# Performance work log

Measured on AMD Instinct MI355X. Metric: run time of the kernel, lower is better.

The kernel has to match this reference:

```python
import jax, jax.numpy as jnp
import numpy as np

HEADS = 16
DIM_HEAD = 64
EPS = 1e-5


def _layernorm(x, w, b):
    mu = jnp.mean(x, axis=-1, keepdims=True)
    var = jnp.var(x, axis=-1, keepdims=True)
    return (x - mu) * jax.lax.rsqrt(var + EPS) * w + b


def setup_inputs() -> dict:
    key = jax.random.key(0)
    ks = jax.random.split(key, 6)
    B, F, Q, D = 8, 4096, 64, 1024
    inner = HEADS * DIM_HEAD  # 1024
    s = 0.02
    return {
        "features": jax.random.normal(ks[0], (B, F, D), jnp.float32),
        "latents": jax.random.normal(ks[1], (B, Q, D), jnp.float32),
        "lnm_w": jnp.ones((D,), jnp.float32),
        "lnm_b": jnp.zeros((D,), jnp.float32),
        "lnl_w": jnp.ones((D,), jnp.float32),
        "lnl_b": jnp.zeros((D,), jnp.float32),
        "Wq": jax.random.normal(ks[2], (D, inner), jnp.float32) * s,
        "Wk": jax.random.normal(ks[3], (D, inner), jnp.float32) * s,
        "Wv": jax.random.normal(ks[4], (D, inner), jnp.float32) * s,
        "Wo": jax.random.normal(ks[5], (inner, D), jnp.float32) * s,
    }


def reference(features, latents, lnm_w, lnm_b, lnl_w, lnl_b, Wq, Wk, Wv, Wo):
    B, Q = latents.shape[0], latents.shape[1]
    scale = DIM_HEAD ** (-0.5)

    x = _layernorm(features, lnm_w, lnm_b)           # (B, F, D)
    lat = _layernorm(latents, lnl_w, lnl_b)          # (B, Q, D)

    q = (lat @ Wq).reshape(B, Q, HEADS, DIM_HEAD).transpose(0, 2, 1, 3)  # b h q d
    kv_in = jnp.concatenate([x, lat], axis=1)        # (B, F+Q, D)
    FL = kv_in.shape[1]
    k = (kv_in @ Wk).reshape(B, FL, HEADS, DIM_HEAD).transpose(0, 2, 1, 3)  # b h f d
    v = (kv_in @ Wv).reshape(B, FL, HEADS, DIM_HEAD).transpose(0, 2, 1, 3)  # b h f d

    sim = jnp.einsum('bhqd,bhfd->bhqf', q * scale, k)
    alphas = jax.nn.softmax(sim, axis=-1)            # amax-subtract is folded into stable softmax
    out = jnp.einsum('bhqf,bhfv->bhqv', alphas, v)
    out = out.transpose(0, 2, 1, 3).reshape(B, Q, HEADS * DIM_HEAD)
    return out @ Wo
```

## Files before the change

kernel.cpp:

```cpp
#include <hip/hip_runtime.h>


typedef float   f32x4  __attribute__((ext_vector_type(4)));
typedef short   bf16x8 __attribute__((ext_vector_type(8)));

#define MFMA_BF16 __builtin_amdgcn_mfma_f32_16x16x32_bf16

__device__ __forceinline__ unsigned short f2bf(float f) {
  unsigned u = __float_as_uint(f);
  unsigned r = (u + 0x7fffu + ((u >> 16) & 1u)) >> 16;
  return (unsigned short)r;
}

__device__ __forceinline__ void gload_lds16(const unsigned short* g, unsigned short* l) {
  __builtin_amdgcn_global_load_lds(
      (const __attribute__((address_space(1))) unsigned int*)g,
      (__attribute__((address_space(3))) unsigned int*)l, 16, 0, 0);
}

__global__ __launch_bounds__(256) void ln_kernel(
    const float* __restrict__ features, const float* __restrict__ latents,
    const float* __restrict__ lnm_w, const float* __restrict__ lnm_b,
    const float* __restrict__ lnl_w, const float* __restrict__ lnl_b,
    unsigned short* __restrict__ kv_ln, unsigned short* __restrict__ lat_ln)
{
  const int row = blockIdx.x;
  const int b  = row / 4160;
  const int fi = row - b * 4160;
  const bool is_lat = fi >= 4096;
  const float* x = is_lat ? (latents + (size_t)(b * 64 + fi - 4096) * 1024)
                          : (features + (size_t)(b * 4096 + fi) * 1024);
  const float* wp = is_lat ? lnl_w : lnm_w;
  const float* bp = is_lat ? lnl_b : lnm_b;
  const int tid = threadIdx.x;

  float4 v = *(const float4*)(x + tid * 4);
  float s  = v.x + v.y + v.z + v.w;
  float s2 = v.x * v.x + v.y * v.y + v.z * v.z + v.w * v.w;
#pragma unroll
  for (int sh = 1; sh < 64; sh <<= 1) {
    s  += __shfl_xor(s,  sh, 64);
    s2 += __shfl_xor(s2, sh, 64);
  }
  __shared__ float red[8];
  if ((tid & 63) == 0) { red[tid >> 6] = s; red[4 + (tid >> 6)] = s2; }
  __syncthreads();
  s  = red[0] + red[1] + red[2] + red[3];
  s2 = red[4] + red[5] + red[6] + red[7];
  const float mu   = s * (1.0f / 1024.0f);
  const float var  = s2 * (1.0f / 1024.0f) - mu * mu;
  const float rstd = rsqrtf(var + 1e-5f);

  float4 w4 = *(const float4*)(wp + tid * 4);
  float4 b4 = *(const float4*)(bp + tid * 4);
  ushort4 o;
  o.x = f2bf((v.x - mu) * rstd * w4.x + b4.x);
  o.y = f2bf((v.y - mu) * rstd * w4.y + b4.y);
  o.z = f2bf((v.z - mu) * rstd * w4.z + b4.z);
  o.w = f2bf((v.w - mu) * rstd * w4.w + b4.w);
  *(ushort4*)(kv_ln + (size_t)row * 1024 + tid * 4) = o;
  if (is_lat)
    *(ushort4*)(lat_ln + (size_t)(b * 64 + fi - 4096) * 1024 + tid * 4) = o;
}

__global__ __launch_bounds__(256) void wcast_kernel(
    const float* __restrict__ Wq, const float* __restrict__ Wk,
    const float* __restrict__ Wv, const float* __restrict__ Wo,
    unsigned short* __restrict__ Wkv_t, unsigned short* __restrict__ Wq_t,
    unsigned short* __restrict__ Wo_t)
{
  __shared__ float tile[32][33];
  const int kt = blockIdx.x * 32, nt = blockIdx.y * 32;
  const int tx = threadIdx.x & 31, ty = threadIdx.x >> 5;

  const float* src; int nc; float scale = 1.0f;
  if (nt < 1024)      { src = Wk; nc = nt; }
  else if (nt < 2048) { src = Wv; nc = nt - 1024; }
  else if (nt < 3072) { src = Wq; nc = nt - 2048; scale = 0.125f; }
  else                { src = Wo; nc = nt - 3072; }

#pragma unroll
  for (int kk = 0; kk < 4; ++kk)
    tile[ty + kk * 8][tx] = src[(size_t)(kt + ty + kk * 8) * 1024 + nc + tx] * scale;
  __syncthreads();

#pragma unroll
  for (int nn = 0; nn < 4; ++nn) {
    const int ng = nt + ty + nn * 8;
    unsigned short* d;
    if (ng < 2048)      d = Wkv_t + (size_t)ng * 1024;
    else if (ng < 3072) d = Wq_t + (size_t)(ng - 2048) * 1024;
    else                d = Wo_t + (size_t)(ng - 3072) * 1024;
    d[kt + tx] = f2bf(tile[tx][ty + nn * 8]);
  }
}

__global__ __launch_bounds__(512, 2) void gemm256_bf16(
    const unsigned short* __restrict__ A,
    const unsigned short* __restrict__ Bt,
    unsigned short* __restrict__ C, int M, int N, int K)
{
  __shared__ __align__(16) unsigned short lds[65536];
  const int tid  = threadIdx.x;
  const int wave = tid >> 6, lane = tid & 63;
  const int lo = lane & 15, hi = lane >> 4;
  const int wr = wave >> 2, wc = wave & 3;

  const int nbn = gridDim.x;
  int flat = blockIdx.y * nbn + blockIdx.x;
  const int nwg = nbn * gridDim.y;
  flat = (flat & 7) * (nwg >> 3) + (flat >> 3);
  const int bm = flat / nbn, bn = flat - bm * nbn;

  int roff[2], coff[2];
#pragma unroll
  for (int g = 0; g < 2; ++g) {
    int off = g * 8192 + tid * 16;
    int p = off ^ (((off >> 9) & 1) << 5);
    int sub = (p >> 10) & 15;
    int q = p & 1023;
    roff[g] = ((sub >> 1) << 4) + (q >> 6);
    coff[g] = ((sub & 1) << 5) + ((q & 63) >> 1);
  }
  const unsigned short* pA[2];
  const unsigned short* pB[2];
#pragma unroll
  for (int g = 0; g < 2; ++g) {
    pA[g] = A  + (size_t)(bm * 256 + roff[g]) * K + coff[g];
    pB[g] = Bt + (size_t)(bn * 256 + roff[g]) * K + coff[g];
  }
  const int halfStep = 128 * K;

  f32x4 acc[8][4];
#pragma unroll
  for (int i = 0; i < 8; ++i)
#pragma unroll
    for (int j = 0; j < 4; ++j) acc[i][j] = (f32x4){0.f, 0.f, 0.f, 0.f};

  const int NT = K >> 6;

#pragma unroll
  for (int ty = 0; ty < 4; ++ty) {
#pragma unroll
    for (int g = 0; g < 2; ++g) {
      const unsigned short* src = (ty == 0) ? pA[g]
                                : (ty == 1) ? pB[g]
                                : (ty == 2) ? pA[g] + halfStep
                                            : pB[g] + halfStep;
      gload_lds16(src, lds + ty * 8192 + g * 4096 + wave * 512);
    }
  }
  asm volatile("s_waitcnt vmcnt(6)" ::: "memory");
  asm volatile("s_barrier" ::: "memory");

  bf16x8 aLo[4][2], aHi[4][2], bLo[2][2], bHi[2][2];
  const int swz = (lo * 32 + hi * 8) ^ ((lo & 8) << 1);

#pragma unroll 2
  for (int t = 0; t < NT; ++t) {
    const unsigned short* sb = lds + (t & 1) * 32768;
    unsigned short*       db = lds + ((t + 1) & 1) * 32768;
    const int k0n = (t + 1) << 6;
    const bool st = (t + 1 < NT);

#pragma unroll
    for (int m = 0; m < 4; ++m)
#pragma unroll
      for (int ks = 0; ks < 2; ++ks)
        aLo[m][ks] = *(const bf16x8*)(sb + ((wr * 4 + m) * 2 + ks) * 512 + swz);
    if (st) {
#pragma unroll
      for (int g = 0; g < 2; ++g)
        gload_lds16(pA[g] + k0n, db + g * 4096 + wave * 512);
    }
    asm volatile("s_barrier" ::: "memory");
    asm volatile("s_waitcnt lgkmcnt(0)" ::: "memory");
    __builtin_amdgcn_sched_barrier(0);
    __builtin_amdgcn_s_setprio(1);
    if (t > 0) {
#pragma unroll
      for (int m = 0; m < 4; ++m)
#pragma unroll
        for (int n = 0; n < 2; ++n)
#pragma unroll
          for (int ks = 0; ks < 2; ++ks)
            acc[4 + m][2 + n] = MFMA_BF16(aHi[m][ks], bHi[n][ks], acc[4 + m][2 + n], 0, 0, 0);
    }
    __builtin_amdgcn_s_setprio(0);
    if (st) { asm volatile("s_waitcnt vmcnt(6)" ::: "memory"); }
    else    { asm volatile("s_waitcnt vmcnt(4)" ::: "memory"); }
    asm volatile("s_barrier" ::: "memory");

#pragma unroll
    for (int n = 0; n < 2; ++n)
#pragma unroll
      for (int ks = 0; ks < 2; ++ks)
        bLo[n][ks] = *(const bf16x8*)(sb + 8192 + ((wc * 2 + n) * 2 + ks) * 512 + swz);
    if (st) {
#pragma unroll
      for (int g = 0; g < 2; ++g)
        gload_lds16(pB[g] + k0n, db + 8192 + g * 4096 + wave * 512);
    }
    asm volatile("s_barrier" ::: "memory");
    asm volatile("s_waitcnt lgkmcnt(0)" ::: "memory");
    __builtin_amdgcn_sched_barrier(0);
    __builtin_amdgcn_s_setprio(1);
#pragma unroll
    for (int m = 0; m < 4; ++m)
#pragma unroll
      for (int n = 0; n < 2; ++n)
#pragma unroll
        for (int ks = 0; ks < 2; ++ks)
          acc[m][n] = MFMA_BF16(aLo[m][ks], bLo[n][ks], acc[m][n], 0, 0, 0);
    __builtin_amdgcn_s_setprio(0);
    if (st) { asm volatile("s_waitcnt vmcnt(6)" ::: "memory"); }
    else    { asm volatile("s_waitcnt vmcnt(2)" ::: "memory"); }
    asm volatile("s_barrier" ::: "memory");

#pragma unroll
    for (int m = 0; m < 4; ++m)
#pragma unroll
      for (int ks = 0; ks < 2; ++ks)
        aHi[m][ks] = *(const bf16x8*)(sb + 16384 + ((wr * 4 + m) * 2 + ks) * 512 + swz);
    if (st) {
#pragma unroll
      for (int g = 0; g < 2; ++g)
        gload_lds16(pA[g] + halfStep + k0n, db + 16384 + g * 4096 + wave * 512);
    }
    asm volatile("s_barrier" ::: "memory");
    asm volatile("s_waitcnt lgkmcnt(0)" ::: "memory");
    __builtin_amdgcn_sched_barrier(0);
    __builtin_amdgcn_s_setprio(1);
#pragma unroll
    for (int m = 0; m < 4; ++m)
#pragma unroll
      for (int n = 0; n < 2; ++n)
#pragma unroll
        for (int ks = 0; ks < 2; ++ks)
          acc[4 + m][n] = MFMA_BF16(aHi[m][ks], bLo[n][ks], acc[4 + m][n], 0, 0, 0);
    __builtin_amdgcn_s_setprio(0);
    if (st) { asm volatile("s_waitcnt vmcnt(6)" ::: "memory"); }
    else    { asm volatile("s_waitcnt vmcnt(0)" ::: "memory"); }
    asm volatile("s_barrier" ::: "memory");

#pragma unroll
    for (int n = 0; n < 2; ++n)
#pragma unroll
      for (int ks = 0; ks < 2; ++ks)
        bHi[n][ks] = *(const bf16x8*)(sb + 24576 + ((wc * 2 + n) * 2 + ks) * 512 + swz);
    if (st) {
#pragma unroll
      for (int g = 0; g < 2; ++g)
        gload_lds16(pB[g] + halfStep + k0n, db + 24576 + g * 4096 + wave * 512);
    }
    asm volatile("s_barrier" ::: "memory");
    asm volatile("s_waitcnt lgkmcnt(0)" ::: "memory");
    __builtin_amdgcn_sched_barrier(0);
    __builtin_amdgcn_s_setprio(1);
#pragma unroll
    for (int m = 0; m < 4; ++m)
#pragma unroll
      for (int n = 0; n < 2; ++n)
#pragma unroll
        for (int ks = 0; ks < 2; ++ks)
          acc[m][2 + n] = MFMA_BF16(aLo[m][ks], bHi[n][ks], acc[m][2 + n], 0, 0, 0);
    __builtin_amdgcn_s_setprio(0);
    if (st) { asm volatile("s_waitcnt vmcnt(6)" ::: "memory"); }
    asm volatile("s_barrier" ::: "memory");
  }

#pragma unroll
  for (int m = 0; m < 4; ++m)
#pragma unroll
    for (int n = 0; n < 2; ++n)
#pragma unroll
      for (int ks = 0; ks < 2; ++ks)
        acc[4 + m][2 + n] = MFMA_BF16(aHi[m][ks], bHi[n][ks], acc[4 + m][2 + n], 0, 0, 0);

#pragma unroll
  for (int i = 0; i < 8; ++i) {
    const int grow0 = bm * 256 + (i >> 2) * 128 + wr * 64 + (i & 3) * 16 + hi * 4;
#pragma unroll
    for (int j = 0; j < 4; ++j) {
      const int gcol = bn * 256 + (j >> 1) * 128 + wc * 32 + (j & 1) * 16 + lo;
#pragma unroll
      for (int r = 0; r < 4; ++r)
        C[(size_t)(grow0 + r) * N + gcol] = f2bf(acc[i][j][r]);
    }
  }
}

template <typename CT>
__global__ __launch_bounds__(256) void gemm_tn(
    const unsigned short* __restrict__ A,
    const unsigned short* __restrict__ Bt,
    CT* __restrict__ C, int M, int N, int K)
{
  __shared__ __align__(16) unsigned short sA[2][128 * 32];
  __shared__ __align__(16) unsigned short sB[2][128 * 32];
  const int tid  = threadIdx.x;
  const int wave = tid >> 6, lane = tid & 63;
  const int bm = blockIdx.y, bn = blockIdx.x;
  const int wr = wave >> 1, wc = wave & 1;
  const int lo = lane & 15, hi = lane >> 4;
  const int srow = lane >> 2, squad = lane & 3;

  const unsigned short* gA = A  + (size_t)(bm * 128 + srow) * K + squad * 8;
  const unsigned short* gB = Bt + (size_t)(bn * 128 + srow) * K + squad * 8;

  f32x4 acc[4][4];
#pragma unroll
  for (int i = 0; i < 4; ++i)
#pragma unroll
    for (int j = 0; j < 4; ++j) acc[i][j] = (f32x4){0.f, 0.f, 0.f, 0.f};

  const int kt = K >> 5;
#pragma unroll
  for (int c = 0; c < 2; ++c) {
    const int chunk = wave * 2 + c;
    gload_lds16(gA + (size_t)chunk * 16 * K, &sA[0][chunk * 512]);
    gload_lds16(gB + (size_t)chunk * 16 * K, &sB[0][chunk * 512]);
  }
  __syncthreads();

  int buf = 0;
  for (int t = 0; t < kt; ++t) {
    if (t + 1 < kt) {
      const int k0 = (t + 1) << 5;
#pragma unroll
      for (int c = 0; c < 2; ++c) {
        const int chunk = wave * 2 + c;
        gload_lds16(gA + (size_t)chunk * 16 * K + k0, &sA[buf ^ 1][chunk * 512]);
        gload_lds16(gB + (size_t)chunk * 16 * K + k0, &sB[buf ^ 1][chunk * 512]);
      }
    }
    bf16x8 af[4], bfr[4];
#pragma unroll
    for (int i = 0; i < 4; ++i) {
      af[i]  = *(const bf16x8*)&sA[buf][(wr * 64 + i * 16 + lo) * 32 + hi * 8];
      bfr[i] = *(const bf16x8*)&sB[buf][(wc * 64 + i * 16 + lo) * 32 + hi * 8];
    }
#pragma unroll
    for (int i = 0; i < 4; ++i)
#pragma unroll
      for (int j = 0; j < 4; ++j)
        acc[i][j] = MFMA_BF16(af[i], bfr[j], acc[i][j], 0, 0, 0);
    __syncthreads();
    buf ^= 1;
  }

#pragma unroll
  for (int i = 0; i < 4; ++i) {
    const int row0 = bm * 128 + wr * 64 + i * 16 + hi * 4;
#pragma unroll
    for (int j = 0; j < 4; ++j) {
      const int col = bn * 128 + wc * 64 + j * 16 + lo;
#pragma unroll
      for (int r = 0; r < 4; ++r) {
        const size_t idx = (size_t)(row0 + r) * N + col;
        if constexpr (sizeof(CT) == 2) C[idx] = (CT)f2bf(acc[i][j][r]);
        else                            C[idx] = acc[i][j][r];
      }
    }
  }
}

__global__ __launch_bounds__(256) void attn_kernel(
    const unsigned short* __restrict__ qws,
    const unsigned short* __restrict__ KV,
    float* __restrict__ pacc, float* __restrict__ pml)
{
  const int bhs = blockIdx.x;
  const int s = bhs & 3, h = (bhs >> 2) & 15, b = bhs >> 6;
  const int t0 = (s * 65) >> 2;
  const int t1 = ((s + 1) * 65) >> 2;
  const int tid = threadIdx.x;
  const int wave = tid >> 6, lane = tid & 63;
  const int lo = lane & 15, hi = lane >> 4;

  __shared__ __align__(16) unsigned short sK [64][72];
  __shared__ __align__(16) unsigned short sVT[64][72];
  __shared__ __align__(16) unsigned short sP [4][16][72];

  bf16x8 qf[2];
  {
    const unsigned short* p = qws + (size_t)(b * 64 + wave * 16 + lo) * 1024 + h * 64 + hi * 8;
    qf[0] = *(const bf16x8*)p;
    qf[1] = *(const bf16x8*)(p + 32);
  }
  float m[4] = {-1e30f, -1e30f, -1e30f, -1e30f};
  float l[4] = {0.f, 0.f, 0.f, 0.f};
  f32x4 acc[4];
#pragma unroll
  for (int i = 0; i < 4; ++i) acc[i] = (f32x4){0.f, 0.f, 0.f, 0.f};

  const int frow = tid >> 2, c4 = tid & 3;

  bf16x8 kreg[2], vreg[2];
  {
    const size_t rb = (size_t)(b * 4160 + t0 * 64 + frow) * 2048 + h * 64;
#pragma unroll
    for (int rr = 0; rr < 2; ++rr) {
      const int d0 = rr * 32 + c4 * 8;
      kreg[rr] = *(const bf16x8*)(KV + rb + d0);
      vreg[rr] = *(const bf16x8*)(KV + rb + 1024 + d0);
    }
  }

  for (int t = t0; t < t1; ++t) {
    __syncthreads();
#pragma unroll
    for (int rr = 0; rr < 2; ++rr) {
      const int d0 = rr * 32 + c4 * 8;
      *(bf16x8*)&sK[frow][d0] = kreg[rr];
#pragma unroll
      for (int j = 0; j < 8; ++j) sVT[d0 + j][frow] = (unsigned short)vreg[rr][j];
    }
    __syncthreads();
    if (t + 1 < t1) {
      const size_t rb = (size_t)(b * 4160 + (t + 1) * 64 + frow) * 2048 + h * 64;
#pragma unroll
      for (int rr = 0; rr < 2; ++rr) {
        const int d0 = rr * 32 + c4 * 8;
        kreg[rr] = *(const bf16x8*)(KV + rb + d0);
        vreg[rr] = *(const bf16x8*)(KV + rb + 1024 + d0);
      }
    }

    f32x4 sim[4];
#pragma unroll
    for (int nf = 0; nf < 4; ++nf) {
      f32x4 a0 = (f32x4){0.f, 0.f, 0.f, 0.f};
#pragma unroll
      for (int ks = 0; ks < 2; ++ks) {
        bf16x8 kf = *(const bf16x8*)&sK[nf * 16 + lo][ks * 32 + hi * 8];
        a0 = MFMA_BF16(qf[ks], kf, a0, 0, 0, 0);
      }
      sim[nf] = a0;
    }

    float pr[4][4];
    float corr[4];
#pragma unroll
    for (int r = 0; r < 4; ++r) {
      float tm = fmaxf(fmaxf(sim[0][r], sim[1][r]), fmaxf(sim[2][r], sim[3][r]));
#pragma unroll
      for (int sh = 1; sh < 16; sh <<= 1) tm = fmaxf(tm, __shfl_xor(tm, sh, 64));
      const float mn = fmaxf(m[r], tm);
      corr[r] = __expf(m[r] - mn);
      float rs = 0.f;
#pragma unroll
      for (int nf = 0; nf < 4; ++nf) {
        float p = __expf(sim[nf][r] - mn);
        pr[r][nf] = p;
        rs += p;
      }
#pragma unroll
      for (int sh = 1; sh < 16; sh <<= 1) rs += __shfl_xor(rs, sh, 64);
      l[r] = l[r] * corr[r] + rs;
      m[r] = mn;
    }

    {
      const int r2 = lane & 3;
      float csel = r2 == 0 ? corr[0] : r2 == 1 ? corr[1] : r2 == 2 ? corr[2] : corr[3];
      const int src = ((lane & 15) >> 2) * 16 + (lane & 3);
      const float cacc = __shfl(csel, src, 64);
#pragma unroll
      for (int i = 0; i < 4; ++i) acc[i] *= cacc;
    }

#pragma unroll
    for (int r = 0; r < 4; ++r)
#pragma unroll
      for (int nf = 0; nf < 4; ++nf)
        sP[wave][hi * 4 + r][nf * 16 + lo] = f2bf(pr[r][nf]);

#pragma unroll
    for (int ks = 0; ks < 2; ++ks) {
      bf16x8 pf = *(const bf16x8*)&sP[wave][lo][ks * 32 + hi * 8];
#pragma unroll
      for (int i = 0; i < 4; ++i) {
        bf16x8 vf = *(const bf16x8*)&sVT[i * 16 + lo][ks * 32 + hi * 8];
        acc[i] = MFMA_BF16(vf, pf, acc[i], 0, 0, 0);
      }
    }
  }

  if (lo == 0) {
#pragma unroll
    for (int r = 0; r < 4; ++r) {
      pml[bhs * 128 + wave * 16 + hi * 4 + r]      = m[r];
      pml[bhs * 128 + 64 + wave * 16 + hi * 4 + r] = l[r];
    }
  }
#pragma unroll
  for (int i = 0; i < 4; ++i)
#pragma unroll
    for (int r = 0; r < 4; ++r)
      pacc[bhs * 4096 + (i * 16 + hi * 4 + r) * 64 + wave * 16 + lo] = acc[i][r];
}

__global__ __launch_bounds__(256) void attn_combine(
    const float* __restrict__ pacc, const float* __restrict__ pml,
    unsigned short* __restrict__ attn_out)
{
  const int bh = blockIdx.x;
  const int b = bh >> 4, h = bh & 15;
  const int t = threadIdx.x;
  const int q = t & 63, dg = t >> 6;
  const int base = bh << 2;

  float mm[4], ll[4];
#pragma unroll
  for (int s = 0; s < 4; ++s) {
    mm[s] = pml[(base + s) * 128 + q];
    ll[s] = pml[(base + s) * 128 + 64 + q];
  }
  float M = fmaxf(fmaxf(mm[0], mm[1]), fmaxf(mm[2], mm[3]));
  float e[4];
  float L = 0.f;
#pragma unroll
  for (int s = 0; s < 4; ++s) { e[s] = __expf(mm[s] - M); L += e[s] * ll[s]; }
  const float inv = 1.0f / L;

#pragma unroll
  for (int dd = 0; dd < 16; ++dd) {
    const int d = dg * 16 + dd;
    float v = 0.f;
#pragma unroll
    for (int s = 0; s < 4; ++s)
      v += e[s] * pacc[(base + s) * 4096 + d * 64 + q];
    attn_out[(size_t)(b * 64 + q) * 1024 + h * 64 + d] = f2bf(v * inv);
  }
}

extern "C" void kernel_launch(void* const* d_in, const int* in_sizes, int n_in,
                              void* d_out, int out_size, void* d_ws, size_t ws_size,
                              hipStream_t stream) {
  const float* features = (const float*)d_in[0];
  const float* latents  = (const float*)d_in[1];
  const float* lnm_w = (const float*)d_in[2];
  const float* lnm_b = (const float*)d_in[3];
  const float* lnl_w = (const float*)d_in[4];
  const float* lnl_b = (const float*)d_in[5];
  const float* Wq = (const float*)d_in[6];
  const float* Wk = (const float*)d_in[7];
  const float* Wv = (const float*)d_in[8];
  const float* Wo = (const float*)d_in[9];
  float* out = (float*)d_out;

  char* ws = (char*)d_ws;
  unsigned short* kv_ln    = (unsigned short*)(ws);
  unsigned short* Wkv_t    = (unsigned short*)(ws + 68157440);
  unsigned short* Wq_t     = (unsigned short*)(ws + 72351744);
  unsigned short* Wo_t     = (unsigned short*)(ws + 74448896);
  unsigned short* lat_ln   = (unsigned short*)(ws + 76546048);
  unsigned short* q_ws     = (unsigned short*)(ws + 77594624);
  unsigned short* attn_out = (unsigned short*)(ws + 78643200);
  unsigned short* KV       = (unsigned short*)(ws + 79691776);
  float* pacc = (float*)(ws);
  float* pml  = (float*)(ws + 8388608);

  ln_kernel<<<33280, 256, 0, stream>>>(features, latents, lnm_w, lnm_b, lnl_w, lnl_b,
                                       kv_ln, lat_ln);
  wcast_kernel<<<dim3(32, 128), 256, 0, stream>>>(Wq, Wk, Wv, Wo, Wkv_t, Wq_t, Wo_t);
  gemm256_bf16<<<dim3(8, 130), 512, 0, stream>>>(kv_ln, Wkv_t, KV, 33280, 2048, 1024);
  gemm_tn<unsigned short><<<dim3(8, 4), 256, 0, stream>>>(lat_ln, Wq_t, q_ws, 512, 1024, 1024);
  attn_kernel<<<512, 256, 0, stream>>>(q_ws, KV, pacc, pml);
  attn_combine<<<128, 256, 0, stream>>>(pacc, pml, attn_out);
  gemm_tn<float><<<dim3(8, 4), 256, 0, stream>>>(attn_out, Wo_t, out, 512, 1024, 1024);
}
```

Baseline: 292.9 us.

## Make KV projection GEMM persistent with per-XCD tile ownership and continuous pipeline

The big KV projection GEMM now launches a fixed grid of 256 persistent workgroups instead of one per output tile. Each workgroup walks a strided sequence of tiles that belong to its XCD, stepping 4 tile-rows at a time. The double-buffered K loop runs straight across tile boundaries, so prefetch of the next tile overlaps the epilogue of the current one. This targets the 1040-tile tail-wave imbalance and the per-tile pipeline ramp, at the cost of more complex indexing and an epilogue store inside the main loop that can stall the pipeline.

After: 294.0 us. About the same (+0.3%).

```diff
diff --git a/kernel.cpp b/kernel.cpp
--- a/kernel.cpp
+++ b/kernel.cpp
@@ -106,30 +106,35 @@
   const int lo = lane & 15, hi = lane >> 4;
   const int wr = wave >> 2, wc = wave & 3;
 
-  const int nbn = gridDim.x;
-  int flat = blockIdx.y * nbn + blockIdx.x;
-  const int nwg = nbn * gridDim.y;
-  flat = (flat & 7) * (nwg >> 3) + (flat >> 3);
-  const int bm = flat / nbn, bn = flat - bm * nbn;
+  const int tilesN = N >> 8;
+  const int perXcd = ((M >> 8) * tilesN) >> 3;
+  const int xcd = blockIdx.x & 7, slot = blockIdx.x >> 3;
+  const int ntw = (perXcd - slot + 31) >> 5;
+  const int KT  = (K >> 6) * ntw;
+
+  int g = xcd * perXcd + slot;
+  int bm = g / tilesN;
+  const int bn = g - bm * tilesN;
 
   int roff[2], coff[2];
 #pragma unroll
-  for (int g = 0; g < 2; ++g) {
-    int off = g * 8192 + tid * 16;
+  for (int gi = 0; gi < 2; ++gi) {
+    int off = gi * 8192 + tid * 16;
     int p = off ^ (((off >> 9) & 1) << 5);
     int sub = (p >> 10) & 15;
     int q = p & 1023;
-    roff[g] = ((sub >> 1) << 4) + (q >> 6);
-    coff[g] = ((sub & 1) << 5) + ((q & 63) >> 1);
+    roff[gi] = ((sub >> 1) << 4) + (q >> 6);
+    coff[gi] = ((sub & 1) << 5) + ((q & 63) >> 1);
   }
   const unsigned short* pA[2];
   const unsigned short* pB[2];
 #pragma unroll
-  for (int g = 0; g < 2; ++g) {
-    pA[g] = A  + (size_t)(bm * 256 + roff[g]) * K + coff[g];
-    pB[g] = Bt + (size_t)(bn * 256 + roff[g]) * K + coff[g];
-  }
-  const int halfStep = 128 * K;
+  for (int gi = 0; gi < 2; ++gi) {
+    pA[gi] = A  + (size_t)(bm * 256 + roff[gi]) * K + coff[gi];
+    pB[gi] = Bt + (size_t)(bn * 256 + roff[gi]) * K + coff[gi];
+  }
+  const int halfStep  = 128 * K;
+  const int tileStepA = 4 * 256 * K;
 
   f32x4 acc[8][4];
 #pragma unroll
@@ -137,17 +142,15 @@
 #pragma unroll
     for (int j = 0; j < 4; ++j) acc[i][j] = (f32x4){0.f, 0.f, 0.f, 0.f};
 
-  const int NT = K >> 6;
-
 #pragma unroll
   for (int ty = 0; ty < 4; ++ty) {
 #pragma unroll
-    for (int g = 0; g < 2; ++g) {
-      const unsigned short* src = (ty == 0) ? pA[g]
-                                : (ty == 1) ? pB[g]
-                                : (ty == 2) ? pA[g] + halfStep
-                                            : pB[g] + halfStep;
-      gload_lds16(src, lds + ty * 8192 + g * 4096 + wave * 512);
+    for (int gi = 0; gi < 2; ++gi) {
+      const unsigned short* src = (ty == 0) ? pA[gi]
+                                : (ty == 1) ? pB[gi]
+                                : (ty == 2) ? pA[gi] + halfStep
+                                            : pB[gi] + halfStep;
+      gload_lds16(src, lds + ty * 8192 + gi * 4096 + wave * 512);
     }
   }
   asm volatile("s_waitcnt vmcnt(6)" ::: "memory");
@@ -156,12 +159,14 @@
   bf16x8 aLo[4][2], aHi[4][2], bLo[2][2], bHi[2][2];
   const int swz = (lo * 32 + hi * 8) ^ ((lo & 8) << 1);
 
-#pragma unroll 2
-  for (int t = 0; t < NT; ++t) {
-    const unsigned short* sb = lds + (t & 1) * 32768;
-    unsigned short*       db = lds + ((t + 1) & 1) * 32768;
-    const int k0n = (t + 1) << 6;
-    const bool st = (t + 1 < NT);
+  for (int kt = 0; kt < KT; ++kt) {
+    const int t_local = kt & 15;
+    const bool bnd = (t_local == 15);
+    const bool st  = (kt + 1 < KT);
+    const unsigned short* sb = lds + (kt & 1) * 32768;
+    unsigned short*       db = lds + ((kt + 1) & 1) * 32768;
+    const int offA = bnd ? tileStepA : ((t_local + 1) << 6);
+    const int offB = bnd ? 0         : ((t_local + 1) << 6);
 
 #pragma unroll
     for (int m = 0; m < 4; ++m)
@@ -170,14 +175,14 @@
         aLo[m][ks] = *(const bf16x8*)(sb + ((wr * 4 + m) * 2 + ks) * 512 + swz);
     if (st) {
 #pragma unroll
-      for (int g = 0; g < 2; ++g)
-        gload_lds16(pA[g] + k0n, db + g * 4096 + wave * 512);
+      for (int gi = 0; gi < 2; ++gi)
+        gload_lds16(pA[gi] + offA, db + gi * 4096 + wave * 512);
     }
     asm volatile("s_barrier" ::: "memory");
     asm volatile("s_waitcnt lgkmcnt(0)" ::: "memory");
     __builtin_amdgcn_sched_barrier(0);
     __builtin_amdgcn_s_setprio(1);
-    if (t > 0) {
+    if (t_local != 0) {
 #pragma unroll
       for (int m = 0; m < 4; ++m)
 #pragma unroll
@@ -198,8 +203,8 @@
         bLo[n][ks] = *(const bf16x8*)(sb + 8192 + ((wc * 2 + n) * 2 + ks) * 512 + swz);
     if (st) {
 #pragma unroll
-      for (int g = 0; g < 2; ++g)
-        gload_lds16(pB[g] + k0n, db + 8192 + g * 4096 + wave * 512);
+      for (int gi = 0; gi < 2; ++gi)
+        gload_lds16(pB[gi] + offB, db + 8192 + gi * 4096 + wave * 512);
     }
     asm volatile("s_barrier" ::: "memory");
     asm volatile("s_waitcnt lgkmcnt(0)" ::: "memory");
@@ -224,8 +229,8 @@
         aHi[m][ks] = *(const bf16x8*)(sb + 16384 + ((wr * 4 + m) * 2 + ks) * 512 + swz);
     if (st) {
 #pragma unroll
-      for (int g = 0; g < 2; ++g)
-        gload_lds16(pA[g] + halfStep + k0n, db + 16384 + g * 4096 + wave * 512);
+      for (int gi = 0; gi < 2; ++gi)
+        gload_lds16(pA[gi] + offA + halfStep, db + 16384 + gi * 4096 + wave * 512);
     }
     asm volatile("s_barrier" ::: "memory");
     asm volatile("s_waitcnt lgkmcnt(0)" ::: "memory");
@@ -250,8 +255,8 @@
         bHi[n][ks] = *(const bf16x8*)(sb + 24576 + ((wc * 2 + n) * 2 + ks) * 512 + swz);
     if (st) {
 #pragma unroll
-      for (int g = 0; g < 2; ++g)
-        gload_lds16(pB[g] + halfStep + k0n, db + 24576 + g * 4096 + wave * 512);
+      for (int gi = 0; gi < 2; ++gi)
+        gload_lds16(pB[gi] + offB + halfStep, db + 24576 + gi * 4096 + wave * 512);
     }
     asm volatile("s_barrier" ::: "memory");
     asm volatile("s_waitcnt lgkmcnt(0)" ::: "memory");
@@ -267,25 +272,35 @@
     __builtin_amdgcn_s_setprio(0);
     if (st) { asm volatile("s_waitcnt vmcnt(6)" ::: "memory"); }
     asm volatile("s_barrier" ::: "memory");
-  }
-
-#pragma unroll
-  for (int m = 0; m < 4; ++m)
-#pragma unroll
-    for (int n = 0; n < 2; ++n)
-#pragma unroll
-      for (int ks = 0; ks < 2; ++ks)
-        acc[4 + m][2 + n] = MFMA_BF16(aHi[m][ks], bHi[n][ks], acc[4 + m][2 + n], 0, 0, 0);
-
-#pragma unroll
-  for (int i = 0; i < 8; ++i) {
-    const int grow0 = bm * 256 + (i >> 2) * 128 + wr * 64 + (i & 3) * 16 + hi * 4;
-#pragma unroll
-    for (int j = 0; j < 4; ++j) {
-      const int gcol = bn * 256 + (j >> 1) * 128 + wc * 32 + (j & 1) * 16 + lo;
-#pragma unroll
-      for (int r = 0; r < 4; ++r)
-        C[(size_t)(grow0 + r) * N + gcol] = f2bf(acc[i][j][r]);
+
+    if (bnd) {
+#pragma unroll
+      for (int m = 0; m < 4; ++m)
+#pragma unroll
+        for (int n = 0; n < 2; ++n)
+#pragma unroll
+          for (int ks = 0; ks < 2; ++ks)
+            acc[4 + m][2 + n] = MFMA_BF16(aHi[m][ks], bHi[n][ks], acc[4 + m][2 + n], 0, 0, 0);
+
+#pragma unroll
+      for (int i = 0; i < 8; ++i) {
+        const int grow0 = bm * 256 + (i >> 2) * 128 + wr * 64 + (i & 3) * 16 + hi * 4;
+#pragma unroll
+        for (int j = 0; j < 4; ++j) {
+          const int gcol = bn * 256 + (j >> 1) * 128 + wc * 32 + (j & 1) * 16 + lo;
+#pragma unroll
+          for (int r = 0; r < 4; ++r)
+            C[(size_t)(grow0 + r) * N + gcol] = f2bf(acc[i][j][r]);
+        }
+      }
+#pragma unroll
+      for (int i = 0; i < 8; ++i)
+#pragma unroll
+        for (int j = 0; j < 4; ++j) acc[i][j] = (f32x4){0.f, 0.f, 0.f, 0.f};
+      if (st) {
+        pA[0] += tileStepA; pA[1] += tileStepA;
+        bm += 4;
+      }
     }
   }
 }
@@ -565,7 +580,7 @@
   ln_kernel<<<33280, 256, 0, stream>>>(features, latents, lnm_w, lnm_b, lnl_w, lnl_b,
                                        kv_ln, lat_ln);
   wcast_kernel<<<dim3(32, 128), 256, 0, stream>>>(Wq, Wk, Wv, Wo, Wkv_t, Wq_t, Wo_t);
-  gemm256_bf16<<<dim3(8, 130), 512, 0, stream>>>(kv_ln, Wkv_t, KV, 33280, 2048, 1024);
+  gemm256_bf16<<<256, 512, 0, stream>>>(kv_ln, Wkv_t, KV, 33280, 2048, 1024);
   gemm_tn<unsigned short><<<dim3(8, 4), 256, 0, stream>>>(lat_ln, Wq_t, q_ws, 512, 1024, 1024);
   attn_kernel<<<512, 256, 0, stream>>>(q_ws, KV, pacc, pml);
   attn_combine<<<128, 256, 0, stream>>>(pacc, pml, attn_out);
```

## Deepen GEMM prefetch, write head-major K/V planes, double attention split

Applied to the files above, without the earlier changes.

The KV projection GEMM now prefetches two K-steps ahead in place and waits on global loads only once per iteration instead of after every quarter-step, aiming to hide more load latency. Its epilogue writes K and V into separate head-major planes, so each attention block streams contiguous 64-wide rows rather than strided 2048-wide rows. The attention kernel splits each (batch, head) into 8 sequence chunks instead of 4, doubling the grid for better occupancy, and the combine kernel merges 8 partials. The risks are overwriting an LDS buffer that is still being read with the in-place prefetch, scattered epilogue stores, and larger partial buffers.

Result: slower. 299.1 us (+2.1%).

```diff
diff --git a/kernel.cpp b/kernel.cpp
--- a/kernel.cpp
+++ b/kernel.cpp
@@ -98,7 +98,8 @@
 __global__ __launch_bounds__(512, 2) void gemm256_bf16(
     const unsigned short* __restrict__ A,
     const unsigned short* __restrict__ Bt,
-    unsigned short* __restrict__ C, int M, int N, int K)
+    unsigned short* __restrict__ Kp, unsigned short* __restrict__ Vp,
+    int M, int N, int K)
 {
   __shared__ __align__(16) unsigned short lds[65536];
   const int tid  = threadIdx.x;
@@ -114,20 +115,20 @@
 
   int roff[2], coff[2];
 #pragma unroll
-  for (int g = 0; g < 2; ++g) {
-    int off = g * 8192 + tid * 16;
+  for (int gi = 0; gi < 2; ++gi) {
+    int off = gi * 8192 + tid * 16;
     int p = off ^ (((off >> 9) & 1) << 5);
     int sub = (p >> 10) & 15;
     int q = p & 1023;
-    roff[g] = ((sub >> 1) << 4) + (q >> 6);
-    coff[g] = ((sub & 1) << 5) + ((q & 63) >> 1);
+    roff[gi] = ((sub >> 1) << 4) + (q >> 6);
+    coff[gi] = ((sub & 1) << 5) + ((q & 63) >> 1);
   }
   const unsigned short* pA[2];
   const unsigned short* pB[2];
 #pragma unroll
-  for (int g = 0; g < 2; ++g) {
-    pA[g] = A  + (size_t)(bm * 256 + roff[g]) * K + coff[g];
-    pB[g] = Bt + (size_t)(bn * 256 + roff[g]) * K + coff[g];
+  for (int gi = 0; gi < 2; ++gi) {
+    pA[gi] = A  + (size_t)(bm * 256 + roff[gi]) * K + coff[gi];
+    pB[gi] = Bt + (size_t)(bn * 256 + roff[gi]) * K + coff[gi];
   }
   const int halfStep = 128 * K;
 
@@ -140,17 +141,19 @@
   const int NT = K >> 6;
 
 #pragma unroll
-  for (int ty = 0; ty < 4; ++ty) {
-#pragma unroll
-    for (int g = 0; g < 2; ++g) {
-      const unsigned short* src = (ty == 0) ? pA[g]
-                                : (ty == 1) ? pB[g]
-                                : (ty == 2) ? pA[g] + halfStep
-                                            : pB[g] + halfStep;
-      gload_lds16(src, lds + ty * 8192 + g * 4096 + wave * 512);
-    }
-  }
-  asm volatile("s_waitcnt vmcnt(6)" ::: "memory");
+  for (int tt = 0; tt < 2; ++tt) {
+    unsigned short* bb = lds + tt * 32768;
+    const int k0 = tt << 6;
+#pragma unroll
+    for (int gi = 0; gi < 2; ++gi) gload_lds16(pA[gi] + k0, bb + gi * 4096 + wave * 512);
+#pragma unroll
+    for (int gi = 0; gi < 2; ++gi) gload_lds16(pB[gi] + k0, bb + 8192 + gi * 4096 + wave * 512);
+#pragma unroll
+    for (int gi = 0; gi < 2; ++gi) gload_lds16(pA[gi] + k0 + halfStep, bb + 16384 + gi * 4096 + wave * 512);
+#pragma unroll
+    for (int gi = 0; gi < 2; ++gi) gload_lds16(pB[gi] + k0 + halfStep, bb + 24576 + gi * 4096 + wave * 512);
+  }
+  asm volatile("s_waitcnt vmcnt(8)" ::: "memory");
   asm volatile("s_barrier" ::: "memory");
 
   bf16x8 aLo[4][2], aHi[4][2], bLo[2][2], bHi[2][2];
@@ -158,10 +161,9 @@
 
 #pragma unroll 2
   for (int t = 0; t < NT; ++t) {
-    const unsigned short* sb = lds + (t & 1) * 32768;
-    unsigned short*       db = lds + ((t + 1) & 1) * 32768;
-    const int k0n = (t + 1) << 6;
-    const bool st = (t + 1 < NT);
+    unsigned short* sb = lds + (t & 1) * 32768;
+    const int k2 = (t + 2) << 6;
+    const bool st = (t + 2 < NT);
 
 #pragma unroll
     for (int m = 0; m < 4; ++m)
@@ -170,8 +172,8 @@
         aLo[m][ks] = *(const bf16x8*)(sb + ((wr * 4 + m) * 2 + ks) * 512 + swz);
     if (st) {
 #pragma unroll
-      for (int g = 0; g < 2; ++g)
-        gload_lds16(pA[g] + k0n, db + g * 4096 + wave * 512);
+      for (int gi = 0; gi < 2; ++gi)
+        gload_lds16(pA[gi] + k2, sb + gi * 4096 + wave * 512);
     }
     asm volatile("s_barrier" ::: "memory");
     asm volatile("s_waitcnt lgkmcnt(0)" ::: "memory");
@@ -187,8 +189,6 @@
             acc[4 + m][2 + n] = MFMA_BF16(aHi[m][ks], bHi[n][ks], acc[4 + m][2 + n], 0, 0, 0);
     }
     __builtin_amdgcn_s_setprio(0);
-    if (st) { asm volatile("s_waitcnt vmcnt(6)" ::: "memory"); }
-    else    { asm volatile("s_waitcnt vmcnt(4)" ::: "memory"); }
     asm volatile("s_barrier" ::: "memory");
 
 #pragma unroll
@@ -198,8 +198,8 @@
         bLo[n][ks] = *(const bf16x8*)(sb + 8192 + ((wc * 2 + n) * 2 + ks) * 512 + swz);
     if (st) {
 #pragma unroll
-      for (int g = 0; g < 2; ++g)
-        gload_lds16(pB[g] + k0n, db + 8192 + g * 4096 + wave * 512);
+      for (int gi = 0; gi < 2; ++gi)
+        gload_lds16(pB[gi] + k2, sb + 8192 + gi * 4096 + wave * 512);
     }
     asm volatile("s_barrier" ::: "memory");
     asm volatile("s_waitcnt lgkmcnt(0)" ::: "memory");
@@ -213,8 +213,6 @@
         for (int ks = 0; ks < 2; ++ks)
           acc[m][n] = MFMA_BF16(aLo[m][ks], bLo[n][ks], acc[m][n], 0, 0, 0);
     __builtin_amdgcn_s_setprio(0);
-    if (st) { asm volatile("s_waitcnt vmcnt(6)" ::: "memory"); }
-    else    { asm volatile("s_waitcnt vmcnt(2)" ::: "memory"); }
     asm volatile("s_barrier" ::: "memory");
 
 #pragma unroll
@@ -224,8 +222,8 @@
         aHi[m][ks] = *(const bf16x8*)(sb + 16384 + ((wr * 4 + m) * 2 + ks) * 512 + swz);
     if (st) {
 #pragma unroll
-      for (int g = 0; g < 2; ++g)
-        gload_lds16(pA[g] + halfStep + k0n, db + 16384 + g * 4096 + wave * 512);
+      for (int gi = 0; gi < 2; ++gi)
+        gload_lds16(pA[gi] + k2 + halfStep, sb + 16384 + gi * 4096 + wave * 512);
     }
     asm volatile("s_barrier" ::: "memory");
     asm volatile("s_waitcnt lgkmcnt(0)" ::: "memory");
@@ -239,8 +237,6 @@
         for (int ks = 0; ks < 2; ++ks)
           acc[4 + m][n] = MFMA_BF16(aHi[m][ks], bLo[n][ks], acc[4 + m][n], 0, 0, 0);
     __builtin_amdgcn_s_setprio(0);
-    if (st) { asm volatile("s_waitcnt vmcnt(6)" ::: "memory"); }
-    else    { asm volatile("s_waitcnt vmcnt(0)" ::: "memory"); }
     asm volatile("s_barrier" ::: "memory");
 
 #pragma unroll
@@ -250,8 +246,8 @@
         bHi[n][ks] = *(const bf16x8*)(sb + 24576 + ((wc * 2 + n) * 2 + ks) * 512 + swz);
     if (st) {
 #pragma unroll
-      for (int g = 0; g < 2; ++g)
-        gload_lds16(pB[g] + halfStep + k0n, db + 24576 + g * 4096 + wave * 512);
+      for (int gi = 0; gi < 2; ++gi)
+        gload_lds16(pB[gi] + k2 + halfStep, sb + 24576 + gi * 4096 + wave * 512);
     }
     asm volatile("s_barrier" ::: "memory");
     asm volatile("s_waitcnt lgkmcnt(0)" ::: "memory");
@@ -265,7 +261,8 @@
         for (int ks = 0; ks < 2; ++ks)
           acc[m][2 + n] = MFMA_BF16(aLo[m][ks], bHi[n][ks], acc[m][2 + n], 0, 0, 0);
     __builtin_amdgcn_s_setprio(0);
-    if (st) { asm volatile("s_waitcnt vmcnt(6)" ::: "memory"); }
+    if (st)                { asm volatile("s_waitcnt vmcnt(6)" ::: "memory"); }
+    else if (t + 1 < NT)   { asm volatile("s_waitcnt vmcnt(0)" ::: "memory"); }
     asm volatile("s_barrier" ::: "memory");
   }
 
@@ -283,9 +280,11 @@
 #pragma unroll
     for (int j = 0; j < 4; ++j) {
       const int gcol = bn * 256 + (j >> 1) * 128 + wc * 32 + (j & 1) * 16 + lo;
+      unsigned short* plane = (gcol & 1024) ? Vp : Kp;
+      const size_t pbase = (size_t)((gcol >> 6) & 15) * 2129920 + (gcol & 63);
 #pragma unroll
       for (int r = 0; r < 4; ++r)
-        C[(size_t)(grow0 + r) * N + gcol] = f2bf(acc[i][j][r]);
+        plane[pbase + (size_t)(grow0 + r) * 64] = f2bf(acc[i][j][r]);
     }
   }
 }
@@ -367,13 +366,13 @@
 
 __global__ __launch_bounds__(256) void attn_kernel(
     const unsigned short* __restrict__ qws,
-    const unsigned short* __restrict__ KV,
+    const unsigned short* __restrict__ Kp, const unsigned short* __restrict__ Vp,
     float* __restrict__ pacc, float* __restrict__ pml)
 {
   const int bhs = blockIdx.x;
-  const int s = bhs & 3, h = (bhs >> 2) & 15, b = bhs >> 6;
-  const int t0 = (s * 65) >> 2;
-  const int t1 = ((s + 1) * 65) >> 2;
+  const int s = bhs & 7, h = (bhs >> 3) & 15, b = bhs >> 7;
+  const int t0 = (s * 65) >> 3;
+  const int t1 = ((s + 1) * 65) >> 3;
   const int tid = threadIdx.x;
   const int wave = tid >> 6, lane = tid & 63;
   const int lo = lane & 15, hi = lane >> 4;
@@ -395,15 +394,16 @@
   for (int i = 0; i < 4; ++i) acc[i] = (f32x4){0.f, 0.f, 0.f, 0.f};
 
   const int frow = tid >> 2, c4 = tid & 3;
+  const size_t hbase = (size_t)h * 2129920;
 
   bf16x8 kreg[2], vreg[2];
   {
-    const size_t rb = (size_t)(b * 4160 + t0 * 64 + frow) * 2048 + h * 64;
+    const size_t rb = hbase + (size_t)(b * 4160 + t0 * 64 + frow) * 64;
 #pragma unroll
     for (int rr = 0; rr < 2; ++rr) {
       const int d0 = rr * 32 + c4 * 8;
-      kreg[rr] = *(const bf16x8*)(KV + rb + d0);
-      vreg[rr] = *(const bf16x8*)(KV + rb + 1024 + d0);
+      kreg[rr] = *(const bf16x8*)(Kp + rb + d0);
+      vreg[rr] = *(const bf16x8*)(Vp + rb + d0);
     }
   }
 
@@ -418,12 +418,12 @@
     }
     __syncthreads();
     if (t + 1 < t1) {
-      const size_t rb = (size_t)(b * 4160 + (t + 1) * 64 + frow) * 2048 + h * 64;
+      const size_t rb = hbase + (size_t)(b * 4160 + (t + 1) * 64 + frow) * 64;
 #pragma unroll
       for (int rr = 0; rr < 2; ++rr) {
         const int d0 = rr * 32 + c4 * 8;
-        kreg[rr] = *(const bf16x8*)(KV + rb + d0);
-        vreg[rr] = *(const bf16x8*)(KV + rb + 1024 + d0);
+        kreg[rr] = *(const bf16x8*)(Kp + rb + d0);
+        vreg[rr] = *(const bf16x8*)(Vp + rb + d0);
       }
     }
 
@@ -509,19 +509,21 @@
   const int b = bh >> 4, h = bh & 15;
   const int t = threadIdx.x;
   const int q = t & 63, dg = t >> 6;
-  const int base = bh << 2;
-
-  float mm[4], ll[4];
-#pragma unroll
-  for (int s = 0; s < 4; ++s) {
+  const int base = bh << 3;
+
+  float mm[8], ll[8];
+#pragma unroll
+  for (int s = 0; s < 8; ++s) {
     mm[s] = pml[(base + s) * 128 + q];
     ll[s] = pml[(base + s) * 128 + 64 + q];
   }
-  float M = fmaxf(fmaxf(mm[0], mm[1]), fmaxf(mm[2], mm[3]));
-  float e[4];
+  float M = mm[0];
+#pragma unroll
+  for (int s = 1; s < 8; ++s) M = fmaxf(M, mm[s]);
+  float e[8];
   float L = 0.f;
 #pragma unroll
-  for (int s = 0; s < 4; ++s) { e[s] = __expf(mm[s] - M); L += e[s] * ll[s]; }
+  for (int s = 0; s < 8; ++s) { e[s] = __expf(mm[s] - M); L += e[s] * ll[s]; }
   const float inv = 1.0f / L;
 
 #pragma unroll
@@ -529,7 +531,7 @@
     const int d = dg * 16 + dd;
     float v = 0.f;
 #pragma unroll
-    for (int s = 0; s < 4; ++s)
+    for (int s = 0; s < 8; ++s)
       v += e[s] * pacc[(base + s) * 4096 + d * 64 + q];
     attn_out[(size_t)(b * 64 + q) * 1024 + h * 64 + d] = f2bf(v * inv);
   }
@@ -558,16 +560,17 @@
   unsigned short* lat_ln   = (unsigned short*)(ws + 76546048);
   unsigned short* q_ws     = (unsigned short*)(ws + 77594624);
   unsigned short* attn_out = (unsigned short*)(ws + 78643200);
-  unsigned short* KV       = (unsigned short*)(ws + 79691776);
+  unsigned short* Kp       = (unsigned short*)(ws + 79691776);
+  unsigned short* Vp       = (unsigned short*)(ws + 147849216);
   float* pacc = (float*)(ws);
-  float* pml  = (float*)(ws + 8388608);
+  float* pml  = (float*)(ws + 16777216);
 
   ln_kernel<<<33280, 256, 0, stream>>>(features, latents, lnm_w, lnm_b, lnl_w, lnl_b,
                                        kv_ln, lat_ln);
   wcast_kernel<<<dim3(32, 128), 256, 0, stream>>>(Wq, Wk, Wv, Wo, Wkv_t, Wq_t, Wo_t);
-  gemm256_bf16<<<dim3(8, 130), 512, 0, stream>>>(kv_ln, Wkv_t, KV, 33280, 2048, 1024);
+  gemm256_bf16<<<dim3(8, 130), 512, 0, stream>>>(kv_ln, Wkv_t, Kp, Vp, 33280, 2048, 1024);
   gemm_tn<unsigned short><<<dim3(8, 4), 256, 0, stream>>>(lat_ln, Wq_t, q_ws, 512, 1024, 1024);
-  attn_kernel<<<512, 256, 0, stream>>>(q_ws, KV, pacc, pml);
+  attn_kernel<<<1024, 256, 0, stream>>>(q_ws, Kp, Vp, pacc, pml);
   attn_combine<<<128, 256, 0, stream>>>(pacc, pml, attn_out);
   gemm_tn<float><<<dim3(8, 4), 256, 0, stream>>>(attn_out, Wo_t, out, 512, 1024, 1024);
 }
```
